# Kernel tuning notes

Measured on AMD Instinct MI355X. Metric: run time of the kernel, lower is better.

The kernel has to match this reference:

```python
import jax, jax.numpy as jnp
import numpy as np

# Sobel kernels stacked as [O=2, I=1, 3, 3]
_KX = np.array([[-1., 0., 1.], [-2., 0., 2.], [-1., 0., 1.]], dtype=np.float32)
_KY = np.array([[1., 2., 1.], [0., 0., 0.], [-1., -2., -1.]], dtype=np.float32)
_SOBEL_W = jnp.asarray(np.stack([_KX, _KY])[:, None, :, :])  # [2,1,3,3]


def _sobel(x):
    # x: [B,1,H,W] -> |Gx| + |Gy| : [B,1,H,W]
    g = jax.lax.conv_general_dilated(
        x, _SOBEL_W, window_strides=(1, 1), padding=((1, 1), (1, 1)),
        dimension_numbers=('NCHW', 'OIHW', 'NCHW'))  # [B,2,H,W]
    return jnp.sum(jnp.abs(g), axis=1, keepdims=True)


def _threshold_mask(g, k):
    # g: [B,1,H,W]; k-th SMALLEST over flattened (C*H*W) per batch (torch.kthvalue)
    B, N, H, W = g.shape
    flat = g.reshape(B, N, H * W)
    kth = jnp.sort(flat, axis=-1)[:, :, k - 1:k]  # [B,N,1]
    mask = (flat >= kth).astype(g.dtype)
    return mask.reshape(B, N, H, W)


def setup_inputs() -> dict:
    key = jax.random.key(0)
    kA, kB, kF = jax.random.split(key, 3)
    shape = (8, 3, 1024, 1024)
    return {
        'image_A': jax.random.uniform(kA, shape, dtype=jnp.float32),
        'image_B': jax.random.uniform(kB, shape, dtype=jnp.float32),
        'image_fused': jax.random.uniform(kF, shape, dtype=jnp.float32),
        'thresholds': 524288,
    }


def reference(image_A, image_B, image_fused, thresholds):
    gA = _sobel(image_A[:, :1])
    gB = _sobel(image_B[:, :1])
    gF = _sobel(image_fused[:, :1])
    joint_max = jnp.maximum(gA, gB)  # max over concat([gA,gB], dim=1) with 1 ch each
    maskA = _threshold_mask(gA, thresholds)
    maskB = _threshold_mask(gB, thresholds)
    loss = jnp.mean(jnp.abs(gF - joint_max))
    return (loss, maskA, maskB)
```

## Files before the change

### kernel.cpp

```cpp
#include <hip/hip_runtime.h>

#define IMG_H 1024
#define IMG_W 1024
#define NBATCH 8
#define NCH 3
#define NPIX (IMG_H * IMG_W)
#define SEGS 64
#define NTOT (8388608LL)

#define BINS1 4096
#define SH1 19

#define WS_MISC_OFF   0
#define WS_MISC_BYTES 4096
#define WS_H1R_OFF    (WS_MISC_OFF + WS_MISC_BYTES)
#define WS_H1R_BYTES  (2 * NBATCH * BINS1 * 4)
#define WS_H1P_OFF    (WS_H1R_OFF + WS_H1R_BYTES)
#define WS_H1P_BYTES  (2 * NBATCH * SEGS * BINS1 * 2)
#define WS_LIST_OFF   (WS_H1P_OFF + WS_H1P_BYTES)

struct Row3f { float l, c, r; };

__device__ __forceinline__ Row3f load3(const float* __restrict__ img, int y, int x) {
    Row3f o;
    if ((unsigned)y >= (unsigned)IMG_H) { o.l = o.c = o.r = 0.0f; return o; }
    const float* row = img + (size_t)y * IMG_W;
    o.c = row[x];
    o.l = (x > 0)         ? row[x - 1] : 0.0f;
    o.r = (x < IMG_W - 1) ? row[x + 1] : 0.0f;
    return o;
}

__device__ __forceinline__ float sobel_g(const Row3f& r0, const Row3f& r1, const Row3f& r2) {
    float gx = r0.r - r0.l;
    gx -= 2.0f * r1.l;
    gx += 2.0f * r1.r;
    gx -= r2.l;
    gx += r2.r;
    float gy = r0.l + 2.0f * r0.c;
    gy += r0.r;
    gy -= r2.l;
    gy -= 2.0f * r2.c;
    gy -= r2.r;
    return fabsf(gx) + fabsf(gy);
}

extern "C" __global__ __launch_bounds__(512)
void k_pass0(const float* __restrict__ A, const float* __restrict__ B,
             const float* __restrict__ F,
             unsigned short* __restrict__ hist1p, double* __restrict__ lossAcc)
{
    __shared__ unsigned int h[4 * BINS1];
    __shared__ double lsum[8];
    const int t = threadIdx.x;
    for (int i = t; i < 4 * BINS1; i += 512) h[i] = 0u;
    __syncthreads();

    const int blk = blockIdx.x;
    const int batch = blk >> 6;
    const int seg = blk & 63;
    const int y0 = (seg >> 1) * 32;
    const int x  = (seg & 1) * 512 + t;
    unsigned int* hc = h + (t >> 8) * (2 * BINS1);

    const float* a = A + (size_t)batch * NCH * NPIX;
    const float* b = B + (size_t)batch * NCH * NPIX;
    const float* f = F + (size_t)batch * NCH * NPIX;

    Row3f a0 = load3(a, y0 - 1, x), a1 = load3(a, y0, x), a2;
    Row3f b0 = load3(b, y0 - 1, x), b1 = load3(b, y0, x), b2;
    Row3f f0 = load3(f, y0 - 1, x), f1 = load3(f, y0, x), f2;

    double loss = 0.0;
    for (int i = 0; i < 32; ++i) {
        const int y = y0 + i;
        a2 = load3(a, y + 1, x);
        b2 = load3(b, y + 1, x);
        f2 = load3(f, y + 1, x);
        const float gA = sobel_g(a0, a1, a2);
        const float gB = sobel_g(b0, b1, b2);
        const float gF = sobel_g(f0, f1, f2);
        atomicAdd(&hc[__float_as_uint(gA) >> SH1], 1u);
        atomicAdd(&hc[BINS1 + (__float_as_uint(gB) >> SH1)], 1u);
        loss += (double)fabsf(gF - fmaxf(gA, gB));
        a0 = a1; a1 = a2;
        b0 = b1; b1 = b2;
        f0 = f1; f1 = f2;
    }
    __syncthreads();

    unsigned short* oA = hist1p + ((size_t)batch            * SEGS + seg) * BINS1;
    unsigned short* oB = hist1p + ((size_t)(NBATCH + batch) * SEGS + seg) * BINS1;
    for (int i = t; i < 2 * BINS1; i += 512) {
        const unsigned v = h[i] + h[2 * BINS1 + i];
        if (i < BINS1) oA[i] = (unsigned short)v;
        else           oB[i - BINS1] = (unsigned short)v;
    }

    for (int off = 32; off > 0; off >>= 1) loss += __shfl_down(loss, off);
    if ((t & 63) == 0) lsum[t >> 6] = loss;
    __syncthreads();
    if (t == 0) {
        double s = 0.0;
        for (int i = 0; i < 8; ++i) s += lsum[i];
        atomicAdd(lossAcc, s);
    }
}

extern "C" __global__ __launch_bounds__(256)
void k_scan1a(const unsigned short* __restrict__ hist1p, unsigned int* __restrict__ hist1r)
{
    const int idx = blockIdx.x * 256 + threadIdx.x;
    const int ib  = idx >> 12;
    const int bin = idx & (BINS1 - 1);
    const unsigned short* p = hist1p + (size_t)ib * SEGS * BINS1 + bin;
    unsigned int s = 0;
    #pragma unroll 8
    for (int sg = 0; sg < SEGS; ++sg) s += p[(size_t)sg * BINS1];
    hist1r[idx] = s;
}

extern "C" __global__ __launch_bounds__(1024)
void k_scan1b(const unsigned int* __restrict__ hist1r, const int* __restrict__ kptr,
              int* __restrict__ sel1, int* __restrict__ resid1)
{
    const int ib = blockIdx.x, t = threadIdx.x;
    const unsigned int* hr = hist1r + (size_t)ib * BINS1;
    long long kl = (long long)kptr[0];
    if (kl < 1 || kl > (long long)NPIX) {
        float kf = ((const float*)kptr)[0];
        kl = (long long)kf;
        if (kl < 1) kl = 1;
        if (kl > NPIX) kl = NPIX;
    }
    const unsigned k = (unsigned)kl;

    const uint4 c = ((const uint4*)hr)[t];
    const unsigned s = c.x + c.y + c.z + c.w;
    __shared__ unsigned ls[1024];
    ls[t] = s; __syncthreads();
    for (int off = 1; off < 1024; off <<= 1) {
        unsigned v = (t >= off) ? ls[t - off] : 0u;
        __syncthreads();
        ls[t] += v;
        __syncthreads();
    }
    const unsigned incl = ls[t];
    const unsigned excl = incl - s;
    if (excl < k && k <= incl) {
        unsigned cum = excl; int bin = t * 4;
        if (cum + c.x < k) { cum += c.x; ++bin;
          if (cum + c.y < k) { cum += c.y; ++bin;
            if (cum + c.z < k) { cum += c.z; ++bin; } } }
        sel1[ib] = bin;
        resid1[ib] = (int)(k - cum);
    }
}

#define PB_ROWS 32
extern "C" __global__ __launch_bounds__(1024)
void k_passB(const float* __restrict__ A, const float* __restrict__ B,
             const int* __restrict__ sel1, unsigned int* __restrict__ gCnt,
             uint2* __restrict__ list, unsigned cap, float* __restrict__ out)
{
    const int t = threadIdx.x;
    const int blk = blockIdx.x;
    const int batch = blk >> 5;
    const int y0 = (blk & 31) * PB_ROWS;
    const int x = t;

    const float* a = A + (size_t)batch * NCH * NPIX;
    const float* b = B + (size_t)batch * NCH * NPIX;
    const unsigned sA = (unsigned)sel1[batch];
    const unsigned sB = (unsigned)sel1[NBATCH + batch];
    float* mA = out + 1 + (size_t)batch * NPIX;
    float* mB = out + 1 + (size_t)NTOT + (size_t)batch * NPIX;

    __shared__ uint2 bufA[2048], bufB[2048];
    __shared__ unsigned cntA, cntB, baseA, baseB;
    if (t == 0) { cntA = 0u; cntB = 0u; }
    __syncthreads();

    Row3f a0 = load3(a, y0 - 1, x), a1 = load3(a, y0, x), a2;
    Row3f b0 = load3(b, y0 - 1, x), b1 = load3(b, y0, x), b2;
    for (int i = 0; i < PB_ROWS; ++i) {
        const int y = y0 + i;
        a2 = load3(a, y + 1, x);
        b2 = load3(b, y + 1, x);
        const unsigned uA = __float_as_uint(sobel_g(a0, a1, a2));
        const unsigned uB = __float_as_uint(sobel_g(b0, b1, b2));
        const unsigned binA = uA >> SH1, binB = uB >> SH1;
        const unsigned idx = (unsigned)y * IMG_W + (unsigned)x;
        mA[idx] = (binA > sA) ? 1.0f : 0.0f;
        mB[idx] = (binB > sB) ? 1.0f : 0.0f;
        if (binA == sA) { unsigned p = atomicAdd(&cntA, 1u); bufA[p] = make_uint2(uA, idx); }
        if (binB == sB) { unsigned p = atomicAdd(&cntB, 1u); bufB[p] = make_uint2(uB, idx); }
        a0 = a1; a1 = a2;
        b0 = b1; b1 = b2;

        __syncthreads();
        const bool last = (i == PB_ROWS - 1);
        const unsigned nA = cntA, nB = cntB;
        const bool doA = (nA >= 1024u) || (last && nA > 0u);
        const bool doB = (nB >= 1024u) || (last && nB > 0u);
        if (doA || doB) {
            if (t == 0) {
                if (doA) baseA = atomicAdd(&gCnt[batch], nA);
                if (doB) baseB = atomicAdd(&gCnt[NBATCH + batch], nB);
            }
            __syncthreads();
            if (doA) {
                const unsigned bs = baseA;
                for (unsigned j = t; j < nA; j += 1024u) {
                    const unsigned d = bs + j;
                    if (d < cap) list[(size_t)batch * cap + d] = bufA[j];
                }
            }
            if (doB) {
                const unsigned bs = baseB;
                for (unsigned j = t; j < nB; j += 1024u) {
                    const unsigned d = bs + j;
                    if (d < cap) list[(size_t)(NBATCH + batch) * cap + d] = bufB[j];
                }
            }
            __syncthreads();
            if (t == 0) { if (doA) cntA = 0u; if (doB) cntB = 0u; }
        }
        __syncthreads();
    }
}

extern "C" __global__ __launch_bounds__(1024)
void k_selectfix(const uint2* __restrict__ list, const unsigned int* __restrict__ gCnt,
                 unsigned cap, const int* __restrict__ sel1, const int* __restrict__ resid1,
                 const double* __restrict__ lossAcc, float* __restrict__ out)
{
    const int ib = blockIdx.x, t = threadIdx.x;
    const unsigned n = min(gCnt[ib], cap);
    const unsigned kk = (unsigned)resid1[ib];
    const uint2* L = list + (size_t)ib * cap;

    __shared__ unsigned h2[BINS1];
    __shared__ unsigned ls[1024];
    __shared__ unsigned bcast[4];
    if (t < 4) bcast[t] = 0u;
    for (int i = t; i < BINS1; i += 1024) h2[i] = 0u;
    __syncthreads();

    for (unsigned j = t; j < n; j += 1024u) atomicAdd(&h2[(L[j].x >> 7) & 4095u], 1u);
    __syncthreads();

    const unsigned c0 = h2[4 * t], c1 = h2[4 * t + 1], c2 = h2[4 * t + 2], c3 = h2[4 * t + 3];
    const unsigned s = c0 + c1 + c2 + c3;
    ls[t] = s; __syncthreads();
    for (int off = 1; off < 1024; off <<= 1) {
        unsigned v = (t >= off) ? ls[t - off] : 0u;
        __syncthreads();
        ls[t] += v;
        __syncthreads();
    }
    {
        const unsigned incl = ls[t], excl = incl - s;
        if (excl < kk && kk <= incl) {
            unsigned cum = excl; unsigned bin = 4u * t;
            if (cum + c0 < kk) { cum += c0; ++bin;
              if (cum + c1 < kk) { cum += c1; ++bin;
                if (cum + c2 < kk) { cum += c2; ++bin; } } }
            bcast[0] = bin;
            bcast[1] = kk - cum;
        }
    }
    __syncthreads();
    const unsigned sel2 = bcast[0], k3 = bcast[1];

    if (t < 128) h2[t] = 0u;
    __syncthreads();
    for (unsigned j = t; j < n; j += 1024u) {
        const unsigned b = L[j].x;
        if (((b >> 7) & 4095u) == sel2) atomicAdd(&h2[b & 127u], 1u);
    }
    __syncthreads();
    {
        const unsigned s3 = (t < 128) ? h2[t] : 0u;
        ls[t] = s3; __syncthreads();
        for (int off = 1; off < 1024; off <<= 1) {
            unsigned v = (t >= off) ? ls[t - off] : 0u;
            __syncthreads();
            ls[t] += v;
            __syncthreads();
        }
        const unsigned incl = ls[t], excl = incl - s3;
        if (t < 128 && excl < k3 && k3 <= incl) {
            bcast[2] = ((unsigned)sel1[ib] << SH1) | (sel2 << 7) | (unsigned)t;
        }
    }
    __syncthreads();
    const unsigned kth = bcast[2];

    float* m = out + 1 + (size_t)ib * NPIX;
    for (unsigned j = t; j < n; j += 1024u) {
        const uint2 e = L[j];
        m[e.y] = (e.x >= kth) ? 1.0f : 0.0f;
    }
    if (ib == 0 && t == 0) out[0] = (float)(lossAcc[0] * (1.0 / 8388608.0));
}

extern "C" void kernel_launch(void* const* d_in, const int* in_sizes, int n_in,
                              void* d_out, int out_size, void* d_ws, size_t ws_size,
                              hipStream_t stream)
{
    const float* A = (const float*)d_in[0];
    const float* B = (const float*)d_in[1];
    const float* F = (const float*)d_in[2];
    const int* kptr = (const int*)d_in[3];
    float* out = (float*)d_out;

    if (ws_size < (size_t)WS_LIST_OFF + 16 * 8 * 1024) return;

    char* ws = (char*)d_ws;
    double* lossAcc        = (double*)(ws + WS_MISC_OFF);
    unsigned int* gCnt     = (unsigned int*)(ws + WS_MISC_OFF + 64);
    unsigned int* hist1r   = (unsigned int*)(ws + WS_H1R_OFF);
    unsigned short* hist1p = (unsigned short*)(ws + WS_H1P_OFF);
    uint2* list            = (uint2*)(ws + WS_LIST_OFF);
    int* sel1              = (int*)(ws + WS_MISC_OFF + 128);
    int* resid1            = (int*)(ws + WS_MISC_OFF + 256);

    unsigned long long capll = (ws_size - WS_LIST_OFF) / (16ull * 8ull);
    unsigned cap = (capll > (unsigned long long)NPIX) ? (unsigned)NPIX : (unsigned)capll;

    hipMemsetAsync(ws, 0, WS_MISC_BYTES, stream);

    k_pass0    <<<dim3(NBATCH * SEGS), dim3(512), 0, stream>>>(A, B, F, hist1p, lossAcc);
    k_scan1a   <<<dim3(2 * NBATCH * BINS1 / 256), dim3(256), 0, stream>>>(hist1p, hist1r);
    k_scan1b   <<<dim3(2 * NBATCH), dim3(1024), 0, stream>>>(hist1r, kptr, sel1, resid1);
    k_passB    <<<dim3(NBATCH * 32), dim3(1024), 0, stream>>>(A, B, sel1, gCnt, list, cap, out);
    k_selectfix<<<dim3(2 * NBATCH), dim3(1024), 0, stream>>>(list, gCnt, cap, sel1, resid1, lossAcc, out);
}
```

Measured before the change: 346.9 us.

## Vectorize sobel rows, fuse histogram scan kernels, use wave-level scans and buffers

Result: slower. 440.6 us (+27.0%).

```diff
diff --git a/kernel.cpp b/kernel.cpp
--- a/kernel.cpp
+++ b/kernel.cpp
@@ -6,6 +6,7 @@
 #define NCH 3
 #define NPIX (IMG_H * IMG_W)
 #define SEGS 64
+#define ROWS_PER_SEG 16
 #define NTOT (8388608LL)
 
 #define BINS1 4096
@@ -13,23 +14,12 @@
 
 #define WS_MISC_OFF   0
 #define WS_MISC_BYTES 4096
-#define WS_H1R_OFF    (WS_MISC_OFF + WS_MISC_BYTES)
-#define WS_H1R_BYTES  (2 * NBATCH * BINS1 * 4)
-#define WS_H1P_OFF    (WS_H1R_OFF + WS_H1R_BYTES)
+#define WS_H1P_OFF    (WS_MISC_OFF + WS_MISC_BYTES)
 #define WS_H1P_BYTES  (2 * NBATCH * SEGS * BINS1 * 2)
 #define WS_LIST_OFF   (WS_H1P_OFF + WS_H1P_BYTES)
 
 struct Row3f { float l, c, r; };
-
-__device__ __forceinline__ Row3f load3(const float* __restrict__ img, int y, int x) {
-    Row3f o;
-    if ((unsigned)y >= (unsigned)IMG_H) { o.l = o.c = o.r = 0.0f; return o; }
-    const float* row = img + (size_t)y * IMG_W;
-    o.c = row[x];
-    o.l = (x > 0)         ? row[x - 1] : 0.0f;
-    o.r = (x < IMG_W - 1) ? row[x + 1] : 0.0f;
-    return o;
-}
+struct Row4  { float l, c0, c1, r; };
 
 __device__ __forceinline__ float sobel_g(const Row3f& r0, const Row3f& r1, const Row3f& r2) {
     float gx = r0.r - r0.l;
@@ -45,6 +35,34 @@
     return fabsf(gx) + fabsf(gy);
 }
 
+__device__ __forceinline__ Row4 load_row2(const float* __restrict__ img, int y, int c0, int lane) {
+    Row4 o;
+    if ((unsigned)y >= (unsigned)IMG_H) { o.l = o.c0 = o.c1 = o.r = 0.0f; return o; }
+    const float* row = img + (size_t)y * IMG_W;
+    const float2 v = *reinterpret_cast<const float2*>(row + c0);
+    float lf = __shfl_up(v.y, 1);
+    float rt = __shfl_down(v.x, 1);
+    if (lane == 0)  lf = (c0 > 0) ? row[c0 - 1] : 0.0f;
+    if (lane == 63) rt = (c0 + 2 < IMG_W) ? row[c0 + 2] : 0.0f;
+    o.l = lf; o.c0 = v.x; o.c1 = v.y; o.r = rt;
+    return o;
+}
+
+__device__ __forceinline__ void sobel2(const Row4& r0, const Row4& r1, const Row4& r2,
+                                       float& g0, float& g1) {
+    g0 = sobel_g(Row3f{r0.l,  r0.c0, r0.c1}, Row3f{r1.l,  r1.c0, r1.c1}, Row3f{r2.l,  r2.c0, r2.c1});
+    g1 = sobel_g(Row3f{r0.c0, r0.c1, r0.r }, Row3f{r1.c0, r1.c1, r1.r }, Row3f{r2.c0, r2.c1, r2.r });
+}
+
+__device__ __forceinline__ unsigned wave_scan(unsigned s, int lane) {
+    #pragma unroll
+    for (int off = 1; off < 64; off <<= 1) {
+        const unsigned v = __shfl_up(s, off);
+        if (lane >= off) s += v;
+    }
+    return s;
+}
+
 extern "C" __global__ __launch_bounds__(512)
 void k_pass0(const float* __restrict__ A, const float* __restrict__ B,
              const float* __restrict__ F,
@@ -53,36 +71,45 @@
     __shared__ unsigned int h[4 * BINS1];
     __shared__ double lsum[8];
     const int t = threadIdx.x;
+    const int lane = t & 63;
     for (int i = t; i < 4 * BINS1; i += 512) h[i] = 0u;
     __syncthreads();
 
     const int blk = blockIdx.x;
     const int batch = blk >> 6;
     const int seg = blk & 63;
-    const int y0 = (seg >> 1) * 32;
-    const int x  = (seg & 1) * 512 + t;
+    const int y0 = seg * ROWS_PER_SEG;
+    const int c0 = 2 * t;
     unsigned int* hc = h + (t >> 8) * (2 * BINS1);
 
     const float* a = A + (size_t)batch * NCH * NPIX;
     const float* b = B + (size_t)batch * NCH * NPIX;
     const float* f = F + (size_t)batch * NCH * NPIX;
 
-    Row3f a0 = load3(a, y0 - 1, x), a1 = load3(a, y0, x), a2;
-    Row3f b0 = load3(b, y0 - 1, x), b1 = load3(b, y0, x), b2;
-    Row3f f0 = load3(f, y0 - 1, x), f1 = load3(f, y0, x), f2;
+    Row4 a0 = load_row2(a, y0 - 1, c0, lane), a1 = load_row2(a, y0, c0, lane), a2;
+    Row4 b0 = load_row2(b, y0 - 1, c0, lane), b1 = load_row2(b, y0, c0, lane), b2;
+    Row4 f0 = load_row2(f, y0 - 1, c0, lane), f1 = load_row2(f, y0, c0, lane), f2;
 
     double loss = 0.0;
-    for (int i = 0; i < 32; ++i) {
+    for (int i = 0; i < ROWS_PER_SEG; ++i) {
         const int y = y0 + i;
-        a2 = load3(a, y + 1, x);
-        b2 = load3(b, y + 1, x);
-        f2 = load3(f, y + 1, x);
-        const float gA = sobel_g(a0, a1, a2);
-        const float gB = sobel_g(b0, b1, b2);
-        const float gF = sobel_g(f0, f1, f2);
-        atomicAdd(&hc[__float_as_uint(gA) >> SH1], 1u);
-        atomicAdd(&hc[BINS1 + (__float_as_uint(gB) >> SH1)], 1u);
-        loss += (double)fabsf(gF - fmaxf(gA, gB));
+        a2 = load_row2(a, y + 1, c0, lane);
+        b2 = load_row2(b, y + 1, c0, lane);
+        f2 = load_row2(f, y + 1, c0, lane);
+        float gA0, gA1, gB0, gB1, gF0, gF1;
+        sobel2(a0, a1, a2, gA0, gA1);
+        sobel2(b0, b1, b2, gB0, gB1);
+        sobel2(f0, f1, f2, gF0, gF1);
+
+        const unsigned bA0 = __float_as_uint(gA0) >> SH1, bA1 = __float_as_uint(gA1) >> SH1;
+        atomicAdd(&hc[bA0], (bA0 == bA1) ? 2u : 1u);
+        if (bA0 != bA1) atomicAdd(&hc[bA1], 1u);
+        const unsigned bB0 = __float_as_uint(gB0) >> SH1, bB1 = __float_as_uint(gB1) >> SH1;
+        atomicAdd(&hc[BINS1 + bB0], (bB0 == bB1) ? 2u : 1u);
+        if (bB0 != bB1) atomicAdd(&hc[BINS1 + bB1], 1u);
+
+        loss += (double)fabsf(gF0 - fmaxf(gA0, gB0));
+        loss += (double)fabsf(gF1 - fmaxf(gA1, gB1));
         a0 = a1; a1 = a2;
         b0 = b1; b1 = b2;
         f0 = f1; f1 = f2;
@@ -98,7 +125,7 @@
     }
 
     for (int off = 32; off > 0; off >>= 1) loss += __shfl_down(loss, off);
-    if ((t & 63) == 0) lsum[t >> 6] = loss;
+    if (lane == 0) lsum[t >> 6] = loss;
     __syncthreads();
     if (t == 0) {
         double s = 0.0;
@@ -107,25 +134,13 @@
     }
 }
 
-extern "C" __global__ __launch_bounds__(256)
-void k_scan1a(const unsigned short* __restrict__ hist1p, unsigned int* __restrict__ hist1r)
-{
-    const int idx = blockIdx.x * 256 + threadIdx.x;
-    const int ib  = idx >> 12;
-    const int bin = idx & (BINS1 - 1);
-    const unsigned short* p = hist1p + (size_t)ib * SEGS * BINS1 + bin;
-    unsigned int s = 0;
-    #pragma unroll 8
-    for (int sg = 0; sg < SEGS; ++sg) s += p[(size_t)sg * BINS1];
-    hist1r[idx] = s;
-}
-
 extern "C" __global__ __launch_bounds__(1024)
-void k_scan1b(const unsigned int* __restrict__ hist1r, const int* __restrict__ kptr,
-              int* __restrict__ sel1, int* __restrict__ resid1)
+void k_select1(const unsigned short* __restrict__ hist1p, const int* __restrict__ kptr,
+               int* __restrict__ sel1, int* __restrict__ resid1)
 {
     const int ib = blockIdx.x, t = threadIdx.x;
-    const unsigned int* hr = hist1r + (size_t)ib * BINS1;
+    const int lane = t & 63, wid = t >> 6;
+
     long long kl = (long long)kptr[0];
     if (kl < 1 || kl > (long long)NPIX) {
         float kf = ((const float*)kptr)[0];
@@ -135,39 +150,66 @@
     }
     const unsigned k = (unsigned)kl;
 
-    const uint4 c = ((const uint4*)hr)[t];
-    const unsigned s = c.x + c.y + c.z + c.w;
-    __shared__ unsigned ls[1024];
-    ls[t] = s; __syncthreads();
-    for (int off = 1; off < 1024; off <<= 1) {
-        unsigned v = (t >= off) ? ls[t - off] : 0u;
-        __syncthreads();
-        ls[t] += v;
-        __syncthreads();
-    }
-    const unsigned incl = ls[t];
+    const ushort4* p = reinterpret_cast<const ushort4*>(hist1p + (size_t)ib * SEGS * BINS1) + t;
+    unsigned c0 = 0, c1 = 0, c2 = 0, c3 = 0;
+    #pragma unroll 4
+    for (int sg = 0; sg < SEGS; ++sg) {
+        const ushort4 v = p[(size_t)sg * (BINS1 / 4)];
+        c0 += v.x; c1 += v.y; c2 += v.z; c3 += v.w;
+    }
+    const unsigned s = c0 + c1 + c2 + c3;
+
+    unsigned incl = wave_scan(s, lane);
+    __shared__ unsigned wsum[16];
+    if (lane == 63) wsum[wid] = incl;
+    __syncthreads();
+    if (wid == 0) {
+        unsigned w = (lane < 16) ? wsum[lane] : 0u;
+        w = wave_scan(w, lane);
+        if (lane < 16) wsum[lane] = w;
+    }
+    __syncthreads();
+    if (wid > 0) incl += wsum[wid - 1];
+
     const unsigned excl = incl - s;
     if (excl < k && k <= incl) {
         unsigned cum = excl; int bin = t * 4;
-        if (cum + c.x < k) { cum += c.x; ++bin;
-          if (cum + c.y < k) { cum += c.y; ++bin;
-            if (cum + c.z < k) { cum += c.z; ++bin; } } }
+        if (cum + c0 < k) { cum += c0; ++bin;
+          if (cum + c1 < k) { cum += c1; ++bin;
+            if (cum + c2 < k) { cum += c2; ++bin; } } }
         sel1[ib] = bin;
         resid1[ib] = (int)(k - cum);
     }
 }
 
-#define PB_ROWS 32
-extern "C" __global__ __launch_bounds__(1024)
+#define PB_BUF   256
+#define PB_FLUSH 128
+
+__device__ __forceinline__ void wave_flush(const uint2* __restrict__ wbuf, unsigned n,
+                                           unsigned int* __restrict__ gcnt,
+                                           uint2* __restrict__ dst, unsigned cap, int lane)
+{
+    __builtin_amdgcn_wave_barrier();
+    unsigned base = 0;
+    if (lane == 0) base = atomicAdd(gcnt, n);
+    base = __shfl(base, 0);
+    for (unsigned j = (unsigned)lane; j < n; j += 64u) {
+        const unsigned d = base + j;
+        if (d < cap) dst[d] = wbuf[j];
+    }
+}
+
+extern "C" __global__ __launch_bounds__(512)
 void k_passB(const float* __restrict__ A, const float* __restrict__ B,
              const int* __restrict__ sel1, unsigned int* __restrict__ gCnt,
              uint2* __restrict__ list, unsigned cap, float* __restrict__ out)
 {
     const int t = threadIdx.x;
+    const int lane = t & 63, wid = t >> 6;
     const int blk = blockIdx.x;
-    const int batch = blk >> 5;
-    const int y0 = (blk & 31) * PB_ROWS;
-    const int x = t;
+    const int batch = blk >> 6;
+    const int y0 = (blk & 63) * ROWS_PER_SEG;
+    const int c0 = 2 * t;
 
     const float* a = A + (size_t)batch * NCH * NPIX;
     const float* b = B + (size_t)batch * NCH * NPIX;
@@ -175,59 +217,67 @@
     const unsigned sB = (unsigned)sel1[NBATCH + batch];
     float* mA = out + 1 + (size_t)batch * NPIX;
     float* mB = out + 1 + (size_t)NTOT + (size_t)batch * NPIX;
-
-    __shared__ uint2 bufA[2048], bufB[2048];
-    __shared__ unsigned cntA, cntB, baseA, baseB;
-    if (t == 0) { cntA = 0u; cntB = 0u; }
-    __syncthreads();
-
-    Row3f a0 = load3(a, y0 - 1, x), a1 = load3(a, y0, x), a2;
-    Row3f b0 = load3(b, y0 - 1, x), b1 = load3(b, y0, x), b2;
-    for (int i = 0; i < PB_ROWS; ++i) {
+    unsigned int* cA = &gCnt[batch];
+    unsigned int* cB = &gCnt[NBATCH + batch];
+    uint2* LA = list + (size_t)batch * cap;
+    uint2* LB = list + (size_t)(NBATCH + batch) * cap;
+
+    __shared__ uint2 buf[8][2][PB_BUF];
+    uint2 (*bufA)[PB_BUF] = &buf[wid][0];
+    uint2 (*bufB)[PB_BUF] = &buf[wid][1];
+    unsigned wcA = 0, wcB = 0;
+
+    Row4 a0 = load_row2(a, y0 - 1, c0, lane), a1 = load_row2(a, y0, c0, lane), a2;
+    Row4 b0 = load_row2(b, y0 - 1, c0, lane), b1 = load_row2(b, y0, c0, lane), b2;
+
+    for (int i = 0; i < ROWS_PER_SEG; ++i) {
         const int y = y0 + i;
-        a2 = load3(a, y + 1, x);
-        b2 = load3(b, y + 1, x);
-        const unsigned uA = __float_as_uint(sobel_g(a0, a1, a2));
-        const unsigned uB = __float_as_uint(sobel_g(b0, b1, b2));
-        const unsigned binA = uA >> SH1, binB = uB >> SH1;
-        const unsigned idx = (unsigned)y * IMG_W + (unsigned)x;
-        mA[idx] = (binA > sA) ? 1.0f : 0.0f;
-        mB[idx] = (binB > sB) ? 1.0f : 0.0f;
-        if (binA == sA) { unsigned p = atomicAdd(&cntA, 1u); bufA[p] = make_uint2(uA, idx); }
-        if (binB == sB) { unsigned p = atomicAdd(&cntB, 1u); bufB[p] = make_uint2(uB, idx); }
+        a2 = load_row2(a, y + 1, c0, lane);
+        b2 = load_row2(b, y + 1, c0, lane);
+        float gA0, gA1, gB0, gB1;
+        sobel2(a0, a1, a2, gA0, gA1);
+        sobel2(b0, b1, b2, gB0, gB1);
+        const unsigned uA0 = __float_as_uint(gA0), uA1 = __float_as_uint(gA1);
+        const unsigned uB0 = __float_as_uint(gB0), uB1 = __float_as_uint(gB1);
+        const unsigned bA0 = uA0 >> SH1, bA1 = uA1 >> SH1;
+        const unsigned bB0 = uB0 >> SH1, bB1 = uB1 >> SH1;
+        const unsigned idx = (unsigned)y * IMG_W + (unsigned)c0;
+
+        *reinterpret_cast<float2*>(mA + idx) =
+            make_float2((bA0 > sA) ? 1.0f : 0.0f, (bA1 > sA) ? 1.0f : 0.0f);
+        *reinterpret_cast<float2*>(mB + idx) =
+            make_float2((bB0 > sB) ? 1.0f : 0.0f, (bB1 > sB) ? 1.0f : 0.0f);
+
+        const unsigned long long lt = ((unsigned long long)1 << lane) - 1ull;
+        {
+            const unsigned long long m0 = __ballot(bA0 == sA);
+            const unsigned long long m1 = __ballot(bA1 == sA);
+            const unsigned n0 = (unsigned)__popcll(m0);
+            const unsigned n01 = n0 + (unsigned)__popcll(m1);
+            if (n01) {
+                if (bA0 == sA) (*bufA)[wcA + (unsigned)__popcll(m0 & lt)] = make_uint2(uA0, idx);
+                if (bA1 == sA) (*bufA)[wcA + n0 + (unsigned)__popcll(m1 & lt)] = make_uint2(uA1, idx + 1);
+                wcA += n01;
+                if (wcA >= PB_FLUSH) { wave_flush(*bufA, wcA, cA, LA, cap, lane); wcA = 0; }
+            }
+        }
+        {
+            const unsigned long long m0 = __ballot(bB0 == sB);
+            const unsigned long long m1 = __ballot(bB1 == sB);
+            const unsigned n0 = (unsigned)__popcll(m0);
+            const unsigned n01 = n0 + (unsigned)__popcll(m1);
+            if (n01) {
+                if (bB0 == sB) (*bufB)[wcB + (unsigned)__popcll(m0 & lt)] = make_uint2(uB0, idx);
+                if (bB1 == sB) (*bufB)[wcB + n0 + (unsigned)__popcll(m1 & lt)] = make_uint2(uB1, idx + 1);
+                wcB += n01;
+                if (wcB >= PB_FLUSH) { wave_flush(*bufB, wcB, cB, LB, cap, lane); wcB = 0; }
+            }
+        }
         a0 = a1; a1 = a2;
         b0 = b1; b1 = b2;
-
-        __syncthreads();
-        const bool last = (i == PB_ROWS - 1);
-        const unsigned nA = cntA, nB = cntB;
-        const bool doA = (nA >= 1024u) || (last && nA > 0u);
-        const bool doB = (nB >= 1024u) || (last && nB > 0u);
-        if (doA || doB) {
-            if (t == 0) {
-                if (doA) baseA = atomicAdd(&gCnt[batch], nA);
-                if (doB) baseB = atomicAdd(&gCnt[NBATCH + batch], nB);
-            }
-            __syncthreads();
-            if (doA) {
-                const unsigned bs = baseA;
-                for (unsigned j = t; j < nA; j += 1024u) {
-                    const unsigned d = bs + j;
-                    if (d < cap) list[(size_t)batch * cap + d] = bufA[j];
-                }
-            }
-            if (doB) {
-                const unsigned bs = baseB;
-                for (unsigned j = t; j < nB; j += 1024u) {
-                    const unsigned d = bs + j;
-                    if (d < cap) list[(size_t)(NBATCH + batch) * cap + d] = bufB[j];
-                }
-            }
-            __syncthreads();
-            if (t == 0) { if (doA) cntA = 0u; if (doB) cntB = 0u; }
-        }
-        __syncthreads();
-    }
+    }
+    if (wcA) wave_flush(*bufA, wcA, cA, LA, cap, lane);
+    if (wcB) wave_flush(*bufB, wcB, cB, LB, cap, lane);
 }
 
 extern "C" __global__ __launch_bounds__(1024)
@@ -236,12 +286,13 @@
                  const double* __restrict__ lossAcc, float* __restrict__ out)
 {
     const int ib = blockIdx.x, t = threadIdx.x;
-    const unsigned n = min(gCnt[ib], cap);
+    const int lane = t & 63, wid = t >> 6;
+    unsigned n = gCnt[ib]; if (n > cap) n = cap;
     const unsigned kk = (unsigned)resid1[ib];
     const uint2* L = list + (size_t)ib * cap;
 
     __shared__ unsigned h2[BINS1];
-    __shared__ unsigned ls[1024];
+    __shared__ unsigned wsum[16];
     __shared__ unsigned bcast[4];
     if (t < 4) bcast[t] = 0u;
     for (int i = t; i < BINS1; i += 1024) h2[i] = 0u;
@@ -252,15 +303,18 @@
 
     const unsigned c0 = h2[4 * t], c1 = h2[4 * t + 1], c2 = h2[4 * t + 2], c3 = h2[4 * t + 3];
     const unsigned s = c0 + c1 + c2 + c3;
-    ls[t] = s; __syncthreads();
-    for (int off = 1; off < 1024; off <<= 1) {
-        unsigned v = (t >= off) ? ls[t - off] : 0u;
-        __syncthreads();
-        ls[t] += v;
-        __syncthreads();
-    }
+    unsigned incl = wave_scan(s, lane);
+    if (lane == 63) wsum[wid] = incl;
+    __syncthreads();
+    if (wid == 0) {
+        unsigned w = (lane < 16) ? wsum[lane] : 0u;
+        w = wave_scan(w, lane);
+        if (lane < 16) wsum[lane] = w;
+    }
+    __syncthreads();
+    if (wid > 0) incl += wsum[wid - 1];
     {
-        const unsigned incl = ls[t], excl = incl - s;
+        const unsigned excl = incl - s;
         if (excl < kk && kk <= incl) {
             unsigned cum = excl; unsigned bin = 4u * t;
             if (cum + c0 < kk) { cum += c0; ++bin;
@@ -276,21 +330,24 @@
     if (t < 128) h2[t] = 0u;
     __syncthreads();
     for (unsigned j = t; j < n; j += 1024u) {
-        const unsigned b = L[j].x;
-        if (((b >> 7) & 4095u) == sel2) atomicAdd(&h2[b & 127u], 1u);
+        const unsigned bbits = L[j].x;
+        if (((bbits >> 7) & 4095u) == sel2) atomicAdd(&h2[bbits & 127u], 1u);
     }
     __syncthreads();
     {
         const unsigned s3 = (t < 128) ? h2[t] : 0u;
-        ls[t] = s3; __syncthreads();
-        for (int off = 1; off < 1024; off <<= 1) {
-            unsigned v = (t >= off) ? ls[t - off] : 0u;
-            __syncthreads();
-            ls[t] += v;
-            __syncthreads();
-        }
-        const unsigned incl = ls[t], excl = incl - s3;
-        if (t < 128 && excl < k3 && k3 <= incl) {
+        unsigned incl3 = wave_scan(s3, lane);
+        if (lane == 63) wsum[wid] = incl3;
+        __syncthreads();
+        if (wid == 0) {
+            unsigned w = (lane < 16) ? wsum[lane] : 0u;
+            w = wave_scan(w, lane);
+            if (lane < 16) wsum[lane] = w;
+        }
+        __syncthreads();
+        if (wid > 0) incl3 += wsum[wid - 1];
+        const unsigned excl3 = incl3 - s3;
+        if (t < 128 && excl3 < k3 && k3 <= incl3) {
             bcast[2] = ((unsigned)sel1[ib] << SH1) | (sel2 << 7) | (unsigned)t;
         }
     }
@@ -320,11 +377,10 @@
     char* ws = (char*)d_ws;
     double* lossAcc        = (double*)(ws + WS_MISC_OFF);
     unsigned int* gCnt     = (unsigned int*)(ws + WS_MISC_OFF + 64);
-    unsigned int* hist1r   = (unsigned int*)(ws + WS_H1R_OFF);
+    int* sel1              = (int*)(ws + WS_MISC_OFF + 128);
+    int* resid1            = (int*)(ws + WS_MISC_OFF + 256);
     unsigned short* hist1p = (unsigned short*)(ws + WS_H1P_OFF);
     uint2* list            = (uint2*)(ws + WS_LIST_OFF);
-    int* sel1              = (int*)(ws + WS_MISC_OFF + 128);
-    int* resid1            = (int*)(ws + WS_MISC_OFF + 256);
 
     unsigned long long capll = (ws_size - WS_LIST_OFF) / (16ull * 8ull);
     unsigned cap = (capll > (unsigned long long)NPIX) ? (unsigned)NPIX : (unsigned)capll;
@@ -332,8 +388,7 @@
     hipMemsetAsync(ws, 0, WS_MISC_BYTES, stream);
 
     k_pass0    <<<dim3(NBATCH * SEGS), dim3(512), 0, stream>>>(A, B, F, hist1p, lossAcc);
-    k_scan1a   <<<dim3(2 * NBATCH * BINS1 / 256), dim3(256), 0, stream>>>(hist1p, hist1r);
-    k_scan1b   <<<dim3(2 * NBATCH), dim3(1024), 0, stream>>>(hist1r, kptr, sel1, resid1);
-    k_passB    <<<dim3(NBATCH * 32), dim3(1024), 0, stream>>>(A, B, sel1, gCnt, list, cap, out);
+    k_select1  <<<dim3(2 * NBATCH), dim3(1024), 0, stream>>>(hist1p, kptr, sel1, resid1);
+    k_passB    <<<dim3(NBATCH * SEGS), dim3(512), 0, stream>>>(A, B, sel1, gCnt, list, cap, out);
     k_selectfix<<<dim3(2 * NBATCH), dim3(1024), 0, stream>>>(list, gCnt, cap, sel1, resid1, lossAcc, out);
 }
```
